# Kernel tuning notes

Measured on AMD Instinct MI355X. Metric: run time of the kernel, lower is better.

Reference implementation:

```python
import jax, jax.numpy as jnp
import numpy as np

N, M, D = 32768, 8192, 256


def setup_inputs() -> dict:
    key = jax.random.key(0)
    kx, ky = jax.random.split(key)
    inputDataX = jax.random.normal(kx, (N, D), dtype=jnp.float32)
    targetDataY = jax.random.normal(ky, (M, D), dtype=jnp.float32)
    dualVariablePsi = jnp.zeros((M,), dtype=jnp.float32)
    return {"inputDataX": inputDataX, "targetDataY": targetDataY, "dualVariablePsi": dualVariablePsi}


def reference(inputDataX, targetDataY, dualVariablePsi):
    # cost[i,j] = 0.5 * ||x_i - y_j||^2, built GEMM-style as in the torch module
    sq_x = jnp.sum(inputDataX ** 2, axis=1, keepdims=True)          # [N, 1]
    sq_y = jnp.sum(targetDataY ** 2, axis=1)[None, :]               # [1, M]
    cross = inputDataX @ targetDataY.T                              # [N, M]
    cost = (sq_x + sq_y - 2.0 * cross) * 0.5
    row_min = jnp.min(cost - dualVariablePsi[None, :], axis=1)      # [N]
    n = inputDataX.shape[0]
    return jnp.sum(row_min) / n + jnp.mean(dualVariablePsi)
```

## Files before the change

### kernel.cpp

```cpp
#include <hip/hip_runtime.h>
#include <hip/hip_bf16.h>
#include <stdint.h>

#define NROWS 32768
#define MCOLS 8192
#define DDIM  256

#define BM 128
#define BN 64
#define NT (MCOLS/BN)
#define NWG (NROWS/BM)

typedef __attribute__((ext_vector_type(8))) int   int8v;
typedef __attribute__((ext_vector_type(4))) int   int4v;
typedef __attribute__((ext_vector_type(4))) float f32x4;

#define AS1 __attribute__((address_space(1)))
#define AS3 __attribute__((address_space(3)))

#define CS_OFF 65536
#define RW_OFF 98304

__device__ __forceinline__ uint32_t pk4_fp8(float4 v) {
  int p = __builtin_amdgcn_cvt_pk_fp8_f32(v.x, v.y, 0, false);
  p = __builtin_amdgcn_cvt_pk_fp8_f32(v.z, v.w, p, true);
  return (uint32_t)p;
}
__device__ __forceinline__ f32x4 vmin4(f32x4 x, f32x4 y) {
  f32x4 r;
  r[0] = fminf(x[0], y[0]); r[1] = fminf(x[1], y[1]);
  r[2] = fminf(x[2], y[2]); r[3] = fminf(x[3], y[3]);
  return r;
}

__global__ void k_prep(const float* __restrict__ X, const float* __restrict__ Y,
                       const float* __restrict__ psi,
                       uint32_t* __restrict__ XqN, uint32_t* __restrict__ Yq,
                       float* __restrict__ xhalf, float* __restrict__ cbuf,
                       float* __restrict__ sum_accum)
{
  const int lane = threadIdx.x & 63;
  const int gw = (blockIdx.x * blockDim.x + threadIdx.x) >> 6;
  const int nw = (gridDim.x * blockDim.x) >> 6;
  for (int row = gw; row < NROWS + MCOLS; row += nw) {
    const bool isX = row < NROWS;
    const int r = isX ? row : row - NROWS;
    const float* src = isX ? (X + (size_t)row * DDIM) : (Y + (size_t)r * DDIM);
    float4 v = ((const float4*)src)[lane];
    const uint32_t pk = pk4_fp8(v);
    if (isX) XqN[(size_t)row * 64 + lane] = pk ^ 0x80808080u;
    else     Yq[(size_t)r * 64 + lane] = pk;
    float s = v.x*v.x + v.y*v.y + v.z*v.z + v.w*v.w;
    #pragma unroll
    for (int m = 32; m >= 1; m >>= 1) s += __shfl_xor(s, m);
    if (lane == 0) {
      if (isX) xhalf[row] = 0.5f * s;
      else     cbuf[r] = 0.5f * s - psi[r];
    }
  }
  if (blockIdx.x == 0 && threadIdx.x == 0) sum_accum[0] = 0.0f;
}

#define STAGE(t_, h_) do {                                                      \
    _Pragma("unroll") for (int _g = 0; _g < 4; ++_g)                            \
      __builtin_amdgcn_global_load_lds(                                         \
          (const AS1 uint32_t*)(srcG[_g] + (size_t)(t_) * 16384),               \
          (AS3 uint32_t*)(ldsB + wbase + (h_) + _g * 1024), 16, 0, 0);          \
  } while (0)

#define ITER(t_, h_) do {                                                       \
    asm volatile("s_waitcnt vmcnt(4)" ::: "memory");                            \
    int8v bf0, bf1;                                                             \
    {                                                                           \
      const char* _b = ldsB + wbase + (h_) + c15 * 256;                         \
      const int4v _l0 = *(const int4v*)(_b + (((w4 * 2 + 0) ^ c15) << 4));      \
      const int4v _h0 = *(const int4v*)(_b + (((w4 * 2 + 1) ^ c15) << 4));      \
      const int4v _l1 = *(const int4v*)(_b + (((8 + w4 * 2 + 0) ^ c15) << 4));  \
      const int4v _h1 = *(const int4v*)(_b + (((8 + w4 * 2 + 1) ^ c15) << 4));  \
      bf0 = (int8v){_l0[0],_l0[1],_l0[2],_l0[3],_h0[0],_h0[1],_h0[2],_h0[3]};   \
      bf1 = (int8v){_l1[0],_l1[1],_l1[2],_l1[3],_h1[0],_h1[1],_h1[2],_h1[3]};   \
    }                                                                           \
    const float cj = *(const float*)(ldsB + CS_OFF + (((t_) * 64) << 2) + cjo); \
    const f32x4 _ci = {cj, cj, cj, cj};                                         \
    f32x4 acc[4];                                                               \
    __builtin_amdgcn_s_setprio(1);                                              \
    _Pragma("unroll") for (int _m = 0; _m < 4; ++_m)                            \
      acc[_m] = __builtin_amdgcn_mfma_scale_f32_16x16x128_f8f6f4(               \
          a[_m][0], bf0, _ci, 0, 0, 0, 0x7F, 0, 0x7F);                          \
    _Pragma("unroll") for (int _m = 0; _m < 4; ++_m)                            \
      acc[_m] = __builtin_amdgcn_mfma_scale_f32_16x16x128_f8f6f4(               \
          a[_m][1], bf1, acc[_m], 0, 0, 0, 0x7F, 0, 0x7F);                      \
    __builtin_amdgcn_s_setprio(0);                                              \
    _Pragma("unroll") for (int _m = 0; _m < 4; ++_m)                            \
      vmin[_m] = vmin4(vmin[_m], acc[_m]);                                      \
    __builtin_amdgcn_sched_barrier(0);                                          \
    if ((t_) + 2 < NT) STAGE((t_) + 2, h_);                                     \
  } while (0)

__global__ __attribute__((amdgpu_flat_work_group_size(512, 512),
                          amdgpu_waves_per_eu(2, 2)))
void k_gemm(const uint32_t* __restrict__ XqN, const uint32_t* __restrict__ Yq,
            const float* __restrict__ cbuf, const float* __restrict__ xhalf,
            float* __restrict__ sum_accum)
{
  __shared__ __align__(16) char ldsB[100352 + 8];

  const int brow = blockIdx.x * BM;
  const int tid  = threadIdx.x;
  const int wid  = tid >> 6;
  const int lane = tid & 63;
  const int rg    = wid >> 2;
  const int strip = wid & 3;
  const int c15 = lane & 15;
  const int w4  = lane >> 4;
  const int wbase = wid * 8192;
  const int cjo = (strip * 16 + c15) << 2;

  int8v a[4][2];
  {
    const char* aBase = (const char*)XqN + ((size_t)(brow + rg * 64 + c15) << 8) + w4 * 32;
    #pragma unroll
    for (int m = 0; m < 4; ++m)
      #pragma unroll
      for (int kc = 0; kc < 2; ++kc)
        a[m][kc] = *(const int8v*)(aBase + m * 4096 + kc * 128);
  }

  const char* srcG[4];
  #pragma unroll
  for (int g = 0; g < 4; ++g) {
    const int cin = 4 * g + (lane >> 4);
    const int col = strip * 16 + cin;
    srcG[g] = (const char*)Yq + (size_t)col * 256 + (((lane & 15) ^ (cin & 15)) << 4);
  }

  #pragma unroll
  for (int g = 0; g < 4; ++g)
    __builtin_amdgcn_global_load_lds(
        (const AS1 uint32_t*)((const char*)cbuf + wid * 4096 + g * 1024 + lane * 16),
        (AS3 uint32_t*)(ldsB + CS_OFF + wid * 4096 + g * 1024), 16, 0, 0);
  STAGE(0, 0);
  STAGE(1, 4096);
  asm volatile("s_waitcnt vmcnt(0)" ::: "memory");
  __builtin_amdgcn_s_barrier();

  f32x4 vmin[4];
  #pragma unroll
  for (int m = 0; m < 4; ++m)
    vmin[m] = (f32x4){3.4e38f, 3.4e38f, 3.4e38f, 3.4e38f};

  #pragma unroll 1
  for (int tt = 0; tt < NT; tt += 2) {
    ITER(tt,     0);
    ITER(tt + 1, 4096);
  }

  float* Rw = (float*)(ldsB + RW_OFF);
  #pragma unroll
  for (int m = 0; m < 4; ++m) {
    #pragma unroll
    for (int r = 0; r < 4; ++r) {
      float v = vmin[m][r];
      v = fminf(v, __shfl_xor(v, 1));
      v = fminf(v, __shfl_xor(v, 2));
      v = fminf(v, __shfl_xor(v, 4));
      v = fminf(v, __shfl_xor(v, 8));
      vmin[m][r] = v;
    }
    if (c15 < 4) {
      float vsel = vmin[m][0];
      vsel = (c15 == 1) ? vmin[m][1] : vsel;
      vsel = (c15 == 2) ? vmin[m][2] : vsel;
      vsel = (c15 == 3) ? vmin[m][3] : vsel;
      Rw[strip * 128 + rg * 64 + m * 16 + w4 * 4 + c15] = vsel;
    }
  }
  __syncthreads();

  float* part = (float*)(ldsB + 100352);
  if (tid < BM) {
    float rm = fminf(fminf(Rw[tid], Rw[128 + tid]),
                     fminf(Rw[256 + tid], Rw[384 + tid]));
    float s = rm + xhalf[brow + tid];
    #pragma unroll
    for (int m = 32; m >= 1; m >>= 1) s += __shfl_xor(s, m);
    if (lane == 0) part[wid] = s;
  }
  __syncthreads();
  if (tid == 0) atomicAdd(sum_accum, part[0] + part[1]);
}

__global__ void k_final(const float* __restrict__ psi, const float* __restrict__ sum_accum,
                        float* __restrict__ out)
{
  __shared__ float sh[4];
  float s = 0.f;
  for (int i = threadIdx.x; i < MCOLS; i += 256) s += psi[i];
  #pragma unroll
  for (int m = 32; m >= 1; m >>= 1) s += __shfl_xor(s, m);
  const int wid = threadIdx.x >> 6, lane = threadIdx.x & 63;
  if (lane == 0) sh[wid] = s;
  __syncthreads();
  if (threadIdx.x == 0)
    out[0] = sum_accum[0] / (float)NROWS + (sh[0] + sh[1] + sh[2] + sh[3]) / (float)MCOLS;
}

extern "C" void kernel_launch(void* const* d_in, const int* in_sizes, int n_in,
                              void* d_out, int out_size, void* d_ws, size_t ws_size,
                              hipStream_t stream)
{
  const float* X   = (const float*)d_in[0];
  const float* Y   = (const float*)d_in[1];
  const float* psi = (const float*)d_in[2];
  float* out = (float*)d_out;

  char* ws = (char*)d_ws;
  uint32_t* XqN    = (uint32_t*)(ws);
  uint32_t* Yq     = (uint32_t*)(ws + (size_t)NROWS * DDIM);
  float* cbuf      = (float*)(ws + (size_t)(NROWS + MCOLS) * DDIM);
  float* xhalf     = (float*)((char*)cbuf + (size_t)MCOLS * 4);
  float* sum_accum = (float*)((char*)xhalf + (size_t)NROWS * 4);

  k_prep <<<2048, 256, 0, stream>>>(X, Y, psi, XqN, Yq, xhalf, cbuf, sum_accum);
  k_gemm <<<NWG, 512, 0, stream>>>(XqN, Yq, cbuf, xhalf, sum_accum);
  k_final<<<1, 256, 0, stream>>>(psi, sum_accum, out);
}
```

Baseline: 78.67 us.

## Double column tile to 128 with 16 waves and register-prefetched column bias

Widens the per-iteration column tile from 64 to 128 and doubles the workgroup to 1024 threads (16 waves, 8 column strips), so each block walks the Y matrix in half as many steps while the loaded X tile is shared across more waves. The column bias is no longer staged through LDS up front. Each lane now loads its own value straight from global memory into a register one tile ahead, which removes the initial LDS fill and its barrier. The loop is peeled so the last two iterations skip staging, and the wait counts are adjusted. This risks higher register and LDS pressure (about 132KB LDS, waves_per_eu 4) and a longer final cross-strip reduction.

```diff
diff --git a/kernel.cpp b/kernel.cpp
--- a/kernel.cpp
+++ b/kernel.cpp
@@ -7,7 +7,7 @@
 #define DDIM  256
 
 #define BM 128
-#define BN 64
+#define BN 128
 #define NT (MCOLS/BN)
 #define NWG (NROWS/BM)
 
@@ -18,8 +18,8 @@
 #define AS1 __attribute__((address_space(1)))
 #define AS3 __attribute__((address_space(3)))
 
-#define CS_OFF 65536
-#define RW_OFF 98304
+#define RW_OFF   131072
+#define PART_OFF 135168
 
 __device__ __forceinline__ uint32_t pk4_fp8(float4 v) {
   int p = __builtin_amdgcn_cvt_pk_fp8_f32(v.x, v.y, 0, false);
@@ -64,12 +64,12 @@
 #define STAGE(t_, h_) do {                                                      \
     _Pragma("unroll") for (int _g = 0; _g < 4; ++_g)                            \
       __builtin_amdgcn_global_load_lds(                                         \
-          (const AS1 uint32_t*)(srcG[_g] + (size_t)(t_) * 16384),               \
+          (const AS1 uint32_t*)(srcG[_g] + (size_t)(t_) * 32768),               \
           (AS3 uint32_t*)(ldsB + wbase + (h_) + _g * 1024), 16, 0, 0);          \
   } while (0)
 
-#define ITER(t_, h_) do {                                                       \
-    asm volatile("s_waitcnt vmcnt(4)" ::: "memory");                            \
+#define ITER(t_, h_, cjv, VM, STG) do {                                         \
+    asm volatile("s_waitcnt " VM ::: "memory");                                 \
     int8v bf0, bf1;                                                             \
     {                                                                           \
       const char* _b = ldsB + wbase + (h_) + c15 * 256;                         \
@@ -80,8 +80,7 @@
       bf0 = (int8v){_l0[0],_l0[1],_l0[2],_l0[3],_h0[0],_h0[1],_h0[2],_h0[3]};   \
       bf1 = (int8v){_l1[0],_l1[1],_l1[2],_l1[3],_h1[0],_h1[1],_h1[2],_h1[3]};   \
     }                                                                           \
-    const float cj = *(const float*)(ldsB + CS_OFF + (((t_) * 64) << 2) + cjo); \
-    const f32x4 _ci = {cj, cj, cj, cj};                                         \
+    const f32x4 _ci = {cjv, cjv, cjv, cjv};                                     \
     f32x4 acc[4];                                                               \
     __builtin_amdgcn_s_setprio(1);                                              \
     _Pragma("unroll") for (int _m = 0; _m < 4; ++_m)                            \
@@ -94,27 +93,26 @@
     _Pragma("unroll") for (int _m = 0; _m < 4; ++_m)                            \
       vmin[_m] = vmin4(vmin[_m], acc[_m]);                                      \
     __builtin_amdgcn_sched_barrier(0);                                          \
-    if ((t_) + 2 < NT) STAGE((t_) + 2, h_);                                     \
+    if (STG) { cjv = cjPtr[((t_) + 2) * BN]; STAGE((t_) + 2, h_); }             \
   } while (0)
 
-__global__ __attribute__((amdgpu_flat_work_group_size(512, 512),
-                          amdgpu_waves_per_eu(2, 2)))
+__global__ __attribute__((amdgpu_flat_work_group_size(1024, 1024),
+                          amdgpu_waves_per_eu(4, 4)))
 void k_gemm(const uint32_t* __restrict__ XqN, const uint32_t* __restrict__ Yq,
             const float* __restrict__ cbuf, const float* __restrict__ xhalf,
             float* __restrict__ sum_accum)
 {
-  __shared__ __align__(16) char ldsB[100352 + 8];
+  __shared__ __align__(16) char ldsB[PART_OFF + 16];
 
   const int brow = blockIdx.x * BM;
   const int tid  = threadIdx.x;
   const int wid  = tid >> 6;
   const int lane = tid & 63;
-  const int rg    = wid >> 2;
-  const int strip = wid & 3;
+  const int rg    = wid >> 3;
+  const int strip = wid & 7;
   const int c15 = lane & 15;
   const int w4  = lane >> 4;
   const int wbase = wid * 8192;
-  const int cjo = (strip * 16 + c15) << 2;
 
   int8v a[4][2];
   {
@@ -131,18 +129,14 @@
   for (int g = 0; g < 4; ++g) {
     const int cin = 4 * g + (lane >> 4);
     const int col = strip * 16 + cin;
-    srcG[g] = (const char*)Yq + (size_t)col * 256 + (((lane & 15) ^ (cin & 15)) << 4);
-  }
-
-  #pragma unroll
-  for (int g = 0; g < 4; ++g)
-    __builtin_amdgcn_global_load_lds(
-        (const AS1 uint32_t*)((const char*)cbuf + wid * 4096 + g * 1024 + lane * 16),
-        (AS3 uint32_t*)(ldsB + CS_OFF + wid * 4096 + g * 1024), 16, 0, 0);
+    srcG[g] = (const char*)Yq + (size_t)col * 256 + (((lane & 15) ^ cin) << 4);
+  }
+  const float* cjPtr = cbuf + strip * 16 + c15;
+
+  float cj0 = cjPtr[0];
   STAGE(0, 0);
+  float cj1 = cjPtr[BN];
   STAGE(1, 4096);
-  asm volatile("s_waitcnt vmcnt(0)" ::: "memory");
-  __builtin_amdgcn_s_barrier();
 
   f32x4 vmin[4];
   #pragma unroll
@@ -150,10 +144,12 @@
     vmin[m] = (f32x4){3.4e38f, 3.4e38f, 3.4e38f, 3.4e38f};
 
   #pragma unroll 1
-  for (int tt = 0; tt < NT; tt += 2) {
-    ITER(tt,     0);
-    ITER(tt + 1, 4096);
-  }
+  for (int tt = 0; tt < NT - 2; tt += 2) {
+    ITER(tt,     0,    cj0, "vmcnt(5)", 1);
+    ITER(tt + 1, 4096, cj1, "vmcnt(5)", 1);
+  }
+  ITER(NT - 2, 0,    cj0, "vmcnt(5)", 0);
+  ITER(NT - 1, 4096, cj1, "vmcnt(0)", 0);
 
   float* Rw = (float*)(ldsB + RW_OFF);
   #pragma unroll
@@ -177,10 +173,11 @@
   }
   __syncthreads();
 
-  float* part = (float*)(ldsB + 100352);
+  float* part = (float*)(ldsB + PART_OFF);
   if (tid < BM) {
-    float rm = fminf(fminf(Rw[tid], Rw[128 + tid]),
-                     fminf(Rw[256 + tid], Rw[384 + tid]));
+    float rm = Rw[tid];
+    #pragma unroll
+    for (int s8 = 1; s8 < 8; ++s8) rm = fminf(rm, Rw[s8 * 128 + tid]);
     float s = rm + xhalf[brow + tid];
     #pragma unroll
     for (int m = 32; m >= 1; m >>= 1) s += __shfl_xor(s, m);
@@ -222,6 +219,6 @@
   float* sum_accum = (float*)((char*)xhalf + (size_t)NROWS * 4);
 
   k_prep <<<2048, 256, 0, stream>>>(X, Y, psi, XqN, Yq, xhalf, cbuf, sum_accum);
-  k_gemm <<<NWG, 512, 0, stream>>>(XqN, Yq, cbuf, xhalf, sum_accum);
+  k_gemm <<<NWG, 1024, 0, stream>>>(XqN, Yq, cbuf, xhalf, sum_accum);
   k_final<<<1, 256, 0, stream>>>(psi, sum_accum, out);
 }
```

Result: slower. 197.4 us (+150.9%).
